# Kernel tuning notes

Measured on AMD Instinct MI355X. Metric: run time of the kernel, lower is better.

Reference implementation:

```python
import jax, jax.numpy as jnp
import numpy as np
import math

DIM = 512
NUM_HEADS = 8
DIM_HEAD = DIM // NUM_HEADS


def normalized_coords(h, w):
    # (h*w, 2) with (x, y) in [0, 1]
    y = jnp.linspace(0.0, 1.0, h)
    x = jnp.linspace(0.0, 1.0, w)
    yg, xg = jnp.meshgrid(y, x, indexing='ij')
    return jnp.stack([xg.ravel(), yg.ravel()], axis=-1)


def rotate_half(x):
    dh = x.shape[-1] // 2
    return jnp.concatenate([-x[..., dh:], x[..., :dh]], axis=-1)


def apply_rope(t, coords):
    # t: (n, heads, seq, dim_head); coords: (seq, 2) (identical across batch)
    dim_half = t.shape[-1] // 2
    freq = 1.0 / (10000.0 ** (jnp.arange(dim_half, dtype=jnp.float32) / dim_half))
    ang_x = coords[:, 0:1] * freq  # (seq, dim_half)
    ang_y = coords[:, 1:2] * freq
    ang = jnp.concatenate([ang_x, ang_y], axis=-1)  # (seq, dim_head)
    cos, sin = jnp.cos(ang), jnp.sin(ang)
    return t * cos + rotate_half(t) * sin


def setup_inputs() -> dict:
    key = jax.random.key(0)
    ks = jax.random.split(key, 12)
    n, Np, d, H, W = 4, 1024, DIM, 64, 64
    s = 0.02
    return {
        'local_feat': jax.random.normal(ks[0], (n, Np, d), jnp.float32),
        'global_feat': jax.random.normal(ks[1], (n, d, H, W), jnp.float32),
        'Wq': jax.random.normal(ks[2], (d, d), jnp.float32) * s,
        'bq': jnp.zeros((d,), jnp.float32),
        'Wk': jax.random.normal(ks[3], (d, d), jnp.float32) * s,
        'bk': jnp.zeros((d,), jnp.float32),
        'Wv': jax.random.normal(ks[4], (d, d), jnp.float32) * s,
        'bv': jnp.zeros((d,), jnp.float32),
        'Wg': jax.random.normal(ks[5], (d, 2 * d), jnp.float32) * s,
        'bg': jnp.zeros((d,), jnp.float32),
        'Wo': jax.random.normal(ks[6], (d, d), jnp.float32) * s,
        'bo': jnp.zeros((d,), jnp.float32),
    }


def reference(local_feat, global_feat, Wq, bq, Wk, bk, Wv, bv, Wg, bg, Wo, bo):
    n, Np, d = local_feat.shape
    _, _, H, W = global_feat.shape
    h, dh = NUM_HEADS, DIM_HEAD
    gf = global_feat.reshape(n, d, H * W).transpose(0, 2, 1)  # (n, HW, d)

    P = int(math.isqrt(Np))
    local_coords = normalized_coords(P, P)      # (Np, 2)
    global_coords = normalized_coords(H, W)     # (HW, 2)

    def proj(x, Wt, b):
        return x @ Wt.T + b

    Q = proj(local_feat, Wq, bq).reshape(n, Np, h, dh).transpose(0, 2, 1, 3)
    K = proj(gf, Wk, bk).reshape(n, H * W, h, dh).transpose(0, 2, 1, 3)
    V = proj(gf, Wv, bv).reshape(n, H * W, h, dh).transpose(0, 2, 1, 3)

    Q = apply_rope(Q, local_coords)
    K = apply_rope(K, global_coords)

    scores = jnp.einsum('bhqd,bhkd->bhqk', Q, K) / math.sqrt(dh)
    attn = jax.nn.softmax(scores, axis=-1)
    ao = jnp.einsum('bhqk,bhkd->bhqd', attn, V)
    ao = ao.transpose(0, 2, 1, 3).reshape(n, Np, d)

    gate = jax.nn.sigmoid(jnp.concatenate([local_feat, ao], axis=-1) @ Wg.T + bg)
    enhanced = local_feat + gate * ao
    return enhanced @ Wo.T + bo
```

## Files before the change

### kernel.cpp

```cpp
#include <hip/hip_runtime.h>
#include <hip/hip_bf16.h>
#include <cstdint>

typedef __hip_bfloat16 BF;
typedef unsigned short ushort_t;
typedef __attribute__((ext_vector_type(8))) __bf16 bf16x8;
typedef __attribute__((ext_vector_type(4))) float f32x4;
typedef __attribute__((ext_vector_type(4))) unsigned uint4v;

__device__ __forceinline__ float bu2f(ushort_t u) {
  return __uint_as_float((unsigned)u << 16);
}
__device__ __forceinline__ unsigned pk2(float a, float b) {
  union { __hip_bfloat162 h; unsigned u; } c;
  c.h = __float22bfloat162_rn(make_float2(a, b));
  return c.u;
}
__device__ __forceinline__ unsigned short f2bu(float f) {
  union { BF b; unsigned short u; } c; c.b = __float2bfloat16(f); return c.u;
}
__device__ __forceinline__ float b2f(BF x) { return __bfloat162float(x); }
__device__ __forceinline__ void rd16f(const float* fp, ushort_t* out) {
#pragma unroll
  for (int j = 0; j < 16; j += 4) {
    float4 v = *(const float4*)(fp + j);
    ((unsigned*)out)[j / 2] = pk2(v.x, v.y);
    ((unsigned*)out)[j / 2 + 1] = pk2(v.z, v.w);
  }
}

#define QS 0.1803368801111f

__global__ __launch_bounds__(256) void prep_k(const float* __restrict__ local,
                                              const float* __restrict__ Wq,
                                              const float* __restrict__ Wk,
                                              const float* __restrict__ Wv,
                                              const float* __restrict__ Wg,
                                              const float* __restrict__ Wo,
                                              BF* __restrict__ localB,
                                              BF* __restrict__ WB) {
  size_t e = ((size_t)blockIdx.x * 256 + threadIdx.x) * 16;
  const float* src;
  BF* dst;
  if (e < 2097152) {
    src = local + e;  dst = localB + e;
  } else {
    size_t f = e - 2097152;
    dst = WB + f;
    if (f < 262144)        src = Wq + f;
    else if (f < 524288)   src = Wk + (f - 262144);
    else if (f < 786432)   src = Wv + (f - 524288);
    else if (f < 1310720)  src = Wg + (f - 786432);
    else                   src = Wo + (f - 1310720);
  }
  ushort_t vals[16];
  rd16f(src, vals);
  *(uint4*)dst = *(uint4*)&vals[0];
  *((uint4*)dst + 1) = *(uint4*)&vals[8];
}

__global__ __launch_bounds__(256) void pre_k(const float* __restrict__ local,
                                             const float* __restrict__ gfeat,
                                             const float* __restrict__ Wq,
                                             const float* __restrict__ bq,
                                             const BF* __restrict__ localB,
                                             const BF* __restrict__ WqB,
                                             BF* __restrict__ gfT,
                                             BF* __restrict__ Qb) {
  __shared__ __align__(16) ushort_t smem[2][64][72];
  const int t = threadIdx.x;
  if (blockIdx.x < 2048) {
    auto T = smem[0];
    const int g = blockIdx.x;
    const int bz = g & 3, mt = (g >> 2) & 63, kt = g >> 8;
    {
      int krow = t >> 2, mg = t & 3;
      ushort_t vals[16];
      rd16f(gfeat + (size_t)bz * 512 * 4096 + (size_t)(kt * 64 + krow) * 4096 +
                mt * 64 + mg * 16,
            vals);
#pragma unroll
      for (int j = 0; j < 16; ++j) T[mg * 16 + j][krow] = vals[j];
    }
    __syncthreads();
    int mrow = t >> 2, kg = t & 3;
    uint4 a = *(const uint4*)&T[mrow][kg * 16];
    uint4 b = *(const uint4*)&T[mrow][kg * 16 + 8];
    size_t o = ((size_t)bz * 4096 + mt * 64 + mrow) * 512 + kt * 64 + kg * 16;
    *(uint4*)&gfT[o] = a;
    *(uint4*)&gfT[o + 8] = b;
    return;
  }
  auto As = smem[0];
  auto Bs = smem[1];
  const int bx = blockIdx.x - 2048;
  const int m0 = (bx & 63) * 64, n0 = (bx >> 6) * 64;
  const int w = t >> 6, lane = t & 63;
  const int quad = lane >> 4, l16 = lane & 15;

  f32x4 acc[4] = {};
  for (int k0 = 0; k0 < 512; k0 += 64) {
    __syncthreads();
    {
      int row = t >> 2, cg = t & 3;
      int kg = k0 + cg * 16;
      if (WqB) {
        const uint4* pa = (const uint4*)(localB + (size_t)(m0 + row) * 512 + kg);
        *(uint4*)&As[row][cg * 16] = pa[0];
        *(uint4*)&As[row][cg * 16 + 8] = pa[1];
        const uint4* pb = (const uint4*)(WqB + (size_t)(n0 + row) * 512 + kg);
        *(uint4*)&Bs[row][cg * 16] = pb[0];
        *(uint4*)&Bs[row][cg * 16 + 8] = pb[1];
      } else {
        ushort_t vals[16];
        rd16f(local + (size_t)(m0 + row) * 512 + kg, vals);
        *(uint4*)&As[row][cg * 16] = *(uint4*)&vals[0];
        *(uint4*)&As[row][cg * 16 + 8] = *(uint4*)&vals[8];
        ushort_t bv[16];
        rd16f(Wq + (size_t)(n0 + row) * 512 + kg, bv);
        *(uint4*)&Bs[row][cg * 16] = *(uint4*)&bv[0];
        *(uint4*)&Bs[row][cg * 16 + 8] = *(uint4*)&bv[8];
      }
    }
    __syncthreads();
#pragma unroll
    for (int kc = 0; kc < 2; ++kc) {
      bf16x8 af = *(const bf16x8*)&As[w * 16 + l16][kc * 32 + quad * 8];
#pragma unroll
      for (int nt = 0; nt < 4; ++nt) {
        bf16x8 bfv = *(const bf16x8*)&Bs[nt * 16 + l16][kc * 32 + quad * 8];
        acc[nt] = __builtin_amdgcn_mfma_f32_16x16x32_bf16(af, bfv, acc[nt], 0, 0, 0);
      }
    }
  }
  const int head = n0 >> 6;
#pragma unroll
  for (int r = 0; r < 4; ++r) {
    int mg = m0 + w * 16 + quad * 4 + r;
    int bb = mg >> 10, qi = mg & 1023;
    float x = (float)(qi & 31) * (1.f / 31.f);
    float y = (float)(qi >> 5) * (1.f / 31.f);
    size_t base = (((size_t)bb * 8 + head) * 1024 + qi) * 64;
#pragma unroll
    for (int j = 0; j < 2; ++j) {
      int c0 = j * 16 + l16;
      float t0 = acc[j][r] + bq[head * 64 + c0];
      float t1 = acc[j + 2][r] + bq[head * 64 + c0 + 32];
      float fr = __expf((float)c0 * (-9.210340371976184f / 32.f));
      float ax = x * fr, ay = y * fr;
      Qb[base + c0] = __float2bfloat16((t0 * __cosf(ax) - t1 * __sinf(ax)) * QS);
      Qb[base + c0 + 32] = __float2bfloat16((t1 * __cosf(ay) + t0 * __sinf(ay)) * QS);
    }
  }
}

__global__ __launch_bounds__(256) void kv_k(const BF* __restrict__ gfT,
                                            const float* __restrict__ Wk,
                                            const float* __restrict__ Wv,
                                            const BF* __restrict__ WkB,
                                            const BF* __restrict__ WvB,
                                            const float* __restrict__ bk,
                                            const float* __restrict__ bv,
                                            BF* __restrict__ Kb,
                                            BF* __restrict__ VTb) {
  __shared__ __align__(16) ushort_t smem[2][128][72];
  auto As = smem[0];
  auto Bs = smem[1];
  const int tid = threadIdx.x;
  const int w = tid >> 6, lane = tid & 63;
  const int quad = lane >> 4, l16 = lane & 15;
  const int wm = w >> 1, wn = w & 1;
  const int g = blockIdx.x;
  const int a = g & 7, y = (g >> 3) & 7, bidx = g >> 6;
  const int m0 = ((bidx << 1) | (a & 1)) * 128;
  const int n0 = y * 128;
  const int bz = a >> 1;

  f32x4 acc[4][4] = {};
  for (int k0 = 0; k0 < 512; k0 += 64) {
    __syncthreads();
#pragma unroll
    for (int u = 0; u < 2; ++u) {
      int unit = tid + u * 256;
      int row = unit >> 2, cg = unit & 3;
      const uint4* p = (const uint4*)(gfT + ((size_t)bz * 4096 + m0 + row) * 512 +
                                      k0 + cg * 16);
      *(uint4*)&As[row][cg * 16] = p[0];
      *(uint4*)&As[row][cg * 16 + 8] = p[1];
    }
    if (WkB) {
      const BF* bb16 = (n0 >= 512) ? WvB : WkB;
      const int nb = (n0 >= 512) ? (n0 - 512) : n0;
#pragma unroll
      for (int u = 0; u < 2; ++u) {
        int unit = tid + u * 256;
        int row = unit >> 2, cg = unit & 3;
        const uint4* p = (const uint4*)(bb16 + (size_t)(nb + row) * 512 +
                                        k0 + cg * 16);
        *(uint4*)&Bs[row][cg * 16] = p[0];
        *(uint4*)&Bs[row][cg * 16 + 8] = p[1];
      }
    } else {
#pragma unroll
      for (int u = 0; u < 2; ++u) {
        int unit = tid + u * 256;
        int row = unit >> 2, cg = unit & 3;
        const float* bsrc = (n0 >= 512) ? Wv : Wk;
        size_t nrow = (n0 >= 512) ? (n0 - 512 + row) : (n0 + row);
        ushort_t vals[16];
        rd16f(bsrc + nrow * 512 + k0 + cg * 16, vals);
        *(uint4*)&Bs[row][cg * 16] = *(uint4*)&vals[0];
        *(uint4*)&Bs[row][cg * 16 + 8] = *(uint4*)&vals[8];
      }
    }
    __syncthreads();
#pragma unroll
    for (int kc = 0; kc < 2; ++kc) {
      bf16x8 af[4], bfv[4];
#pragma unroll
      for (int i = 0; i < 4; ++i) {
        af[i] = *(const bf16x8*)&As[wm * 64 + i * 16 + l16][kc * 32 + quad * 8];
        bfv[i] = *(const bf16x8*)&Bs[wn * 64 + i * 16 + l16][kc * 32 + quad * 8];
      }
#pragma unroll
      for (int mt = 0; mt < 4; ++mt)
#pragma unroll
        for (int nt = 0; nt < 4; ++nt)
          acc[mt][nt] = __builtin_amdgcn_mfma_f32_16x16x32_bf16(af[mt], bfv[nt], acc[mt][nt], 0, 0, 0);
    }
  }
  if (n0 < 512) {
    const int head = (n0 + wn * 64) >> 6;
#pragma unroll
    for (int mt = 0; mt < 4; ++mt)
#pragma unroll
      for (int r = 0; r < 4; ++r) {
        int pg = m0 + wm * 64 + mt * 16 + quad * 4 + r;
        float x = (float)(pg & 63) * (1.f / 63.f);
        float yy = (float)(pg >> 6) * (1.f / 63.f);
        size_t base = (((size_t)bz * 8 + head) * 4096 + pg) * 64;
#pragma unroll
        for (int j = 0; j < 2; ++j) {
          int c0 = j * 16 + l16;
          float t0 = acc[mt][j][r] + bk[head * 64 + c0];
          float t1 = acc[mt][j + 2][r] + bk[head * 64 + c0 + 32];
          float fr = __expf((float)c0 * (-9.210340371976184f / 32.f));
          float ax = x * fr, ay = yy * fr;
          Kb[base + c0] = __float2bfloat16(t0 * __cosf(ax) - t1 * __sinf(ax));
          Kb[base + c0 + 32] = __float2bfloat16(t1 * __cosf(ay) + t0 * __sinf(ay));
        }
      }
  } else {
    const int n0v = n0 - 512;
    __syncthreads();
    ushort_t (*T)[136] = (ushort_t(*)[136]) & smem[0][0][0];
#pragma unroll
    for (int mt = 0; mt < 4; ++mt)
#pragma unroll
      for (int nt = 0; nt < 4; ++nt)
#pragma unroll
        for (int r = 0; r < 4; ++r) {
          int n_l = wn * 64 + nt * 16 + l16;
          int m_l = wm * 64 + mt * 16 + quad * 4 + r;
          T[n_l][m_l] = f2bu(acc[mt][nt][r] + bv[n0v + n_l]);
        }
    __syncthreads();
    int row = tid >> 1, half = tid & 1;
    size_t gbase = (((size_t)bz * 8 + (n0v >> 6) + (row >> 6)) * 64 + (row & 63)) * 4096 +
                   m0 + half * 64;
    uint4* dst = (uint4*)(VTb + gbase);
    const uint4* src = (const uint4*)&T[row][half * 64];
#pragma unroll
    for (int j = 0; j < 8; ++j) dst[j] = src[j];
  }
}

template <int NS>
__global__ __launch_bounds__(256, 4) void attn_k(const BF* __restrict__ Q,
                                                 const BF* __restrict__ K,
                                                 const BF* __restrict__ VT,
                                                 BF* __restrict__ AO,
                                                 BF* __restrict__ Opart,
                                                 float* __restrict__ lpart) {
  __shared__ __align__(16) ushort_t Ks[2][64][64];
  __shared__ __align__(16) ushort_t VTs[2][64][64];

  const int tid = threadIdx.x;
  const int w = tid >> 6, lane = tid & 63;
  const int quad = lane >> 4, l16 = lane & 15;
  const int r3 = l16 & 7;
  const int sc0 = (quad ^ r3) << 3;
  const int sc1 = sc0 ^ 32;

  const int g = blockIdx.x;
  const int bh = g & 31;
  const int qt = (g >> 5) & 7;
  const int ks = g >> 8;
  const int b = bh >> 3, h = bh & 7;
  const int q0 = qt * 128 + w * 32;
  const int kspan = 4096 / NS, kbase = ks * kspan;

  bf16x8 qa[2][2];
#pragma unroll
  for (int qs = 0; qs < 2; ++qs) {
    const BF* qp = Q + (((size_t)bh << 10) + q0 + qs * 16 + l16) * 64 + quad * 8;
    qa[qs][0] = *(const bf16x8*)qp;
    qa[qs][1] = *(const bf16x8*)(qp + 32);
  }
  bf16x8 ones;
#pragma unroll
  for (int j = 0; j < 8; ++j) ones[j] = (__bf16)1.0f;

  const BF* Kp = K + (size_t)bh * 4096 * 64;
  const BF* VTp = VT + (size_t)bh * 64 * 4096;

  f32x4 o[2][4] = {};
  f32x4 ol[2] = {};

  const int srow = tid >> 2, scol = (tid & 3) * 16;
  const int ssc = ((2 * (tid & 3)) ^ (srow & 7)) << 3;
  int vcol[4];
  {
    const int s1 = (tid >> 1) & 1, s0v = tid & 1;
#pragma unroll
    for (int gq = 0; gq < 4; ++gq)
      vcol[gq] = (((s1 * 4 + gq) ^ (srow & 7)) << 3) + s0v * 4;
  }

#define STAGE_V(buf, v0, v1)                                   \
  {                                                            \
    uint2 t_;                                                  \
    t_.x = (v0).x; t_.y = (v0).y; *(uint2*)&VTs[buf][srow][vcol[0]] = t_; \
    t_.x = (v0).z; t_.y = (v0).w; *(uint2*)&VTs[buf][srow][vcol[1]] = t_; \
    t_.x = (v1).x; t_.y = (v1).y; *(uint2*)&VTs[buf][srow][vcol[2]] = t_; \
    t_.x = (v1).z; t_.y = (v1).w; *(uint2*)&VTs[buf][srow][vcol[3]] = t_; \
  }

  {
    const uint4* kp = (const uint4*)(Kp + (size_t)(kbase + srow) * 64 + scol);
    const uint4* vp = (const uint4*)(VTp + (size_t)srow * 4096 + kbase + scol);
    uint4 a = kp[0], bb = kp[1], c = vp[0], d = vp[1];
    *(uint4*)&Ks[0][srow][ssc] = a;  *(uint4*)&Ks[0][srow][ssc ^ 8] = bb;
    STAGE_V(0, c, d);
  }
  __syncthreads();

  const int nc = kspan / 64;
  for (int c = 0; c < nc; ++c) {
    const int cur = c & 1;
    uint4 nk0, nk1, nv0, nv1;
    const bool more = (c + 1 < nc);
    if (more) {
      const int c1 = kbase + (c + 1) * 64;
      const uint4* kp = (const uint4*)(Kp + (size_t)(c1 + srow) * 64 + scol);
      const uint4* vp = (const uint4*)(VTp + (size_t)srow * 4096 + c1 + scol);
      nk0 = kp[0]; nk1 = kp[1]; nv0 = vp[0]; nv1 = vp[1];
    }

    unsigned pa_u[2][2][4];
#pragma unroll
    for (int ct = 0; ct < 4; ++ct) {
      const int krow = ct * 16 + l16;
      bf16x8 kb0 = *(const bf16x8*)&Ks[cur][krow][sc0];
      bf16x8 kb1 = *(const bf16x8*)&Ks[cur][krow][sc1];
#pragma unroll
      for (int qs = 0; qs < 2; ++qs) {
        f32x4 s = {};
        __builtin_amdgcn_s_setprio(1);
        s = __builtin_amdgcn_mfma_f32_16x16x32_bf16(kb0, qa[qs][0], s, 0, 0, 0);
        s = __builtin_amdgcn_mfma_f32_16x16x32_bf16(kb1, qa[qs][1], s, 0, 0, 0);
        __builtin_amdgcn_s_setprio(0);
        pa_u[qs][ct >> 1][(ct & 1) * 2] =
            pk2(__builtin_exp2f(s[0]), __builtin_exp2f(s[1]));
        pa_u[qs][ct >> 1][(ct & 1) * 2 + 1] =
            pk2(__builtin_exp2f(s[2]), __builtin_exp2f(s[3]));
      }
    }
    bf16x8 pa[2][2];
#pragma unroll
    for (int qs = 0; qs < 2; ++qs)
#pragma unroll
      for (int kk = 0; kk < 2; ++kk) {
        uint4v u = {pa_u[qs][kk][0], pa_u[qs][kk][1], pa_u[qs][kk][2],
                    pa_u[qs][kk][3]};
        pa[qs][kk] = __builtin_bit_cast(bf16x8, u);
      }

    __builtin_amdgcn_s_setprio(1);
#pragma unroll
    for (int qs = 0; qs < 2; ++qs) {
      ol[qs] = __builtin_amdgcn_mfma_f32_16x16x32_bf16(ones, pa[qs][0], ol[qs], 0, 0, 0);
      ol[qs] = __builtin_amdgcn_mfma_f32_16x16x32_bf16(ones, pa[qs][1], ol[qs], 0, 0, 0);
    }
#pragma unroll
    for (int nt = 0; nt < 4; ++nt) {
      const int vrow = nt * 16 + l16;
      bf16x8 vb0 = *(const bf16x8*)&VTs[cur][vrow][sc0];
      bf16x8 vb1 = *(const bf16x8*)&VTs[cur][vrow][sc1];
#pragma unroll
      for (int qs = 0; qs < 2; ++qs) {
        o[qs][nt] = __builtin_amdgcn_mfma_f32_16x16x32_bf16(vb0, pa[qs][0], o[qs][nt], 0, 0, 0);
        o[qs][nt] = __builtin_amdgcn_mfma_f32_16x16x32_bf16(vb1, pa[qs][1], o[qs][nt], 0, 0, 0);
      }
    }
    __builtin_amdgcn_s_setprio(0);

    if (more) {
      *(uint4*)&Ks[cur ^ 1][srow][ssc] = nk0;
      *(uint4*)&Ks[cur ^ 1][srow][ssc ^ 8] = nk1;
      STAGE_V(cur ^ 1, nv0, nv1);
    }
    __syncthreads();
  }
#undef STAGE_V

#pragma unroll
  for (int qs = 0; qs < 2; ++qs) {
    int qg = q0 + qs * 16 + l16;
    if (NS == 1) {
      float invl = 1.f / ol[qs][0];
#pragma unroll
      for (int nt = 0; nt < 4; ++nt) {
        uint2 uu;
        uu.x = pk2(o[qs][nt][0] * invl, o[qs][nt][1] * invl);
        uu.y = pk2(o[qs][nt][2] * invl, o[qs][nt][3] * invl);
        *(uint2*)(AO + (((size_t)b << 10) + qg) * 512 + h * 64 + nt * 16 + quad * 4) = uu;
      }
    } else {
      if (quad == 0) lpart[ks * 32768 + (bh << 10) + qg] = ol[qs][0];
#pragma unroll
      for (int nt = 0; nt < 4; ++nt) {
        uint2 uu;
        uu.x = pk2(o[qs][nt][0], o[qs][nt][1]);
        uu.y = pk2(o[qs][nt][2], o[qs][nt][3]);
        *(uint2*)(Opart + (size_t)ks * 2097152 + (((size_t)bh << 10) + qg) * 64 +
                  nt * 16 + quad * 4) = uu;
      }
    }
  }
}

template <int NS>
__global__ __launch_bounds__(256) void gate_k(const float* __restrict__ local,
                                              const BF* __restrict__ localB,
                                              const BF* __restrict__ AO,
                                              const BF* __restrict__ Opart,
                                              const float* __restrict__ lpart,
                                              const float* __restrict__ Wg,
                                              const BF* __restrict__ WgB,
                                              const float* __restrict__ bg,
                                              BF* __restrict__ ENH) {
  __shared__ __align__(16) ushort_t As[64][72];
  __shared__ __align__(16) ushort_t Bs[64][72];
  const int tid = threadIdx.x;
  const int w = tid >> 6, lane = tid & 63;
  const int quad = lane >> 4, l16 = lane & 15;
  const int m0 = blockIdx.x * 64, n0 = blockIdx.y * 64;

  f32x4 acc[4] = {};
  float aosv[4][4];
  for (int k0 = 0; k0 < 1024; k0 += 64) {
    __syncthreads();
    {
      int row = tid >> 2, cg = tid & 3;
      int kg = k0 + cg * 16;
      ushort_t vals[16];
      if (kg < 512) {
        if (localB) {
          const uint4* p = (const uint4*)(localB + (size_t)(m0 + row) * 512 + kg);
          *(uint4*)&vals[0] = p[0]; *(uint4*)&vals[8] = p[1];
        } else {
          rd16f(local + (size_t)(m0 + row) * 512 + kg, vals);
        }
      } else {
        int c = kg - 512;
        int hh = c >> 6, dh0 = c & 63;
        int mg = m0 + row;
        size_t bq = (size_t)(((mg >> 10) * 8 + hh) << 10) + (mg & 1023);
        if (NS == 1) {
          const uint4* p = (const uint4*)(AO + (size_t)mg * 512 + c);
          *(uint4*)&vals[0] = p[0]; *(uint4*)&vals[8] = p[1];
        } else {
          float ls = 0.f;
#pragma unroll
          for (int s2 = 0; s2 < NS; ++s2) ls += lpart[s2 * 32768 + bq];
          float inv = 1.f / ls;
          float av[16] = {};
#pragma unroll
          for (int s2 = 0; s2 < NS; ++s2) {
            const ushort_t* op = (const ushort_t*)Opart + (size_t)s2 * 2097152 +
                                 bq * 64 + dh0;
            uint4 u0 = ((const uint4*)op)[0], u1 = ((const uint4*)op)[1];
            const ushort_t* pu = (const ushort_t*)&u0;
#pragma unroll
            for (int j = 0; j < 8; ++j) av[j] += bu2f(pu[j]);
            pu = (const ushort_t*)&u1;
#pragma unroll
            for (int j = 0; j < 8; ++j) av[8 + j] += bu2f(pu[j]);
          }
#pragma unroll
          for (int j = 0; j < 16; j += 2)
            ((unsigned*)vals)[j / 2] = pk2(av[j] * inv, av[j + 1] * inv);
        }
      }
      *(uint4*)&As[row][cg * 16] = *(uint4*)&vals[0];
      *(uint4*)&As[row][cg * 16 + 8] = *(uint4*)&vals[8];
      if (WgB) {
        const uint4* p = (const uint4*)(WgB + (size_t)(n0 + row) * 1024 + kg);
        *(uint4*)&Bs[row][cg * 16] = p[0];
        *(uint4*)&Bs[row][cg * 16 + 8] = p[1];
      } else {
        ushort_t bv[16];
        rd16f(Wg + (size_t)(n0 + row) * 1024 + kg, bv);
        *(uint4*)&Bs[row][cg * 16] = *(uint4*)&bv[0];
        *(uint4*)&Bs[row][cg * 16 + 8] = *(uint4*)&bv[8];
      }
    }
    __syncthreads();
    if (k0 == 512 + n0) {
#pragma unroll
      for (int r = 0; r < 4; ++r)
#pragma unroll
        for (int nt = 0; nt < 4; ++nt)
          aosv[r][nt] = bu2f(As[w * 16 + quad * 4 + r][nt * 16 + l16]);
    }
#pragma unroll
    for (int kc = 0; kc < 2; ++kc) {
      bf16x8 af = *(const bf16x8*)&As[w * 16 + l16][kc * 32 + quad * 8];
#pragma unroll
      for (int nt = 0; nt < 4; ++nt) {
        bf16x8 bfv = *(const bf16x8*)&Bs[nt * 16 + l16][kc * 32 + quad * 8];
        acc[nt] = __builtin_amdgcn_mfma_f32_16x16x32_bf16(af, bfv, acc[nt], 0, 0, 0);
      }
    }
  }
#pragma unroll
  for (int r = 0; r < 4; ++r) {
    int mg = m0 + w * 16 + quad * 4 + r;
#pragma unroll
    for (int nt = 0; nt < 4; ++nt) {
      int ng = n0 + nt * 16 + l16;
      size_t idx = (size_t)mg * 512 + ng;
      float gg = 1.f / (1.f + __expf(-(acc[nt][r] + bg[ng])));
      ENH[idx] = __float2bfloat16(local[idx] + gg * aosv[r][nt]);
    }
  }
}

__global__ __launch_bounds__(256) void out_k(const BF* __restrict__ ENH,
                                             const float* __restrict__ Wo,
                                             const BF* __restrict__ WoB,
                                             const float* __restrict__ bo,
                                             float* __restrict__ out) {
  __shared__ __align__(16) ushort_t As[64][72];
  __shared__ __align__(16) ushort_t Bs[64][72];
  const int tid = threadIdx.x;
  const int w = tid >> 6, lane = tid & 63;
  const int quad = lane >> 4, l16 = lane & 15;
  const int m0 = blockIdx.x * 64, n0 = blockIdx.y * 64;

  f32x4 acc[4] = {};
  for (int k0 = 0; k0 < 512; k0 += 64) {
    __syncthreads();
    {
      int row = tid >> 2, cg = tid & 3;
      int kg = k0 + cg * 16;
      const uint4* p = (const uint4*)(ENH + (size_t)(m0 + row) * 512 + kg);
      *(uint4*)&As[row][cg * 16] = p[0];
      *(uint4*)&As[row][cg * 16 + 8] = p[1];
      if (WoB) {
        const uint4* pb = (const uint4*)(WoB + (size_t)(n0 + row) * 512 + kg);
        *(uint4*)&Bs[row][cg * 16] = pb[0];
        *(uint4*)&Bs[row][cg * 16 + 8] = pb[1];
      } else {
        ushort_t bv[16];
        rd16f(Wo + (size_t)(n0 + row) * 512 + kg, bv);
        *(uint4*)&Bs[row][cg * 16] = *(uint4*)&bv[0];
        *(uint4*)&Bs[row][cg * 16 + 8] = *(uint4*)&bv[8];
      }
    }
    __syncthreads();
#pragma unroll
    for (int kc = 0; kc < 2; ++kc) {
      bf16x8 af = *(const bf16x8*)&As[w * 16 + l16][kc * 32 + quad * 8];
#pragma unroll
      for (int nt = 0; nt < 4; ++nt) {
        bf16x8 bfv = *(const bf16x8*)&Bs[nt * 16 + l16][kc * 32 + quad * 8];
        acc[nt] = __builtin_amdgcn_mfma_f32_16x16x32_bf16(af, bfv, acc[nt], 0, 0, 0);
      }
    }
  }
#pragma unroll
  for (int r = 0; r < 4; ++r) {
    int mg = m0 + w * 16 + quad * 4 + r;
#pragma unroll
    for (int nt = 0; nt < 4; ++nt) {
      int ng = n0 + nt * 16 + l16;
      out[(size_t)mg * 512 + ng] = acc[nt][r] + bo[ng];
    }
  }
}

extern "C" void kernel_launch(void* const* d_in, const int* in_sizes, int n_in,
                              void* d_out, int out_size, void* d_ws, size_t ws_size,
                              hipStream_t stream) {
  const float* local = (const float*)d_in[0];
  const float* gfeat = (const float*)d_in[1];
  const float* Wq = (const float*)d_in[2];
  const float* bq = (const float*)d_in[3];
  const float* Wk = (const float*)d_in[4];
  const float* bk = (const float*)d_in[5];
  const float* Wv = (const float*)d_in[6];
  const float* bv = (const float*)d_in[7];
  const float* Wg = (const float*)d_in[8];
  const float* bg = (const float*)d_in[9];
  const float* Wo = (const float*)d_in[10];
  const float* bo = (const float*)d_in[11];

  char* w = (char*)d_ws;
  BF* Qb = (BF*)w;            w += (size_t)2097152 * 2;
  BF* Kb = (BF*)w;            w += (size_t)8388608 * 2;
  BF* VTb = (BF*)w;           w += (size_t)8388608 * 2;
  BF* AO = (BF*)w;            w += (size_t)2097152 * 2;
  BF* gfT = (BF*)w;
  BF* Opart = (BF*)w;
  size_t baseOff = (size_t)(w - (char*)d_ws);
  BF* ENH = Qb;

  int NS = 1;
  if (baseOff + 4 * (4194304 + 131072) <= ws_size) NS = 4;
  else if (baseOff + 16777216 + 2 * 131072 <= ws_size) NS = 2;
  float* lpart = (float*)(w + (size_t)NS * 4194304);

  size_t xsize = (size_t)NS * (4194304 + 131072);
  if (xsize < 16777216) xsize = 16777216;
  BF* WB = (BF*)(w + xsize);
  BF* localB = WB + 1572864;
  bool useP = (baseOff + xsize + 3145728 + 4194304) <= ws_size;
  const BF *WqB = nullptr, *WkB = nullptr, *WvB = nullptr, *WgB = nullptr,
           *WoB = nullptr, *locB = nullptr;
  if (useP) {
    WqB = WB;            WkB = WB + 262144;  WvB = WB + 524288;
    WgB = WB + 786432;   WoB = WB + 1310720; locB = localB;
  }

  dim3 blk(256);
  if (useP)
    prep_k<<<dim3(896), blk, 0, stream>>>(local, Wq, Wk, Wv, Wg, Wo, localB, WB);
  pre_k<<<dim3(2560), blk, 0, stream>>>(local, gfeat, Wq, bq, locB, WqB, gfT, Qb);
  kv_k<<<dim3(1024), blk, 0, stream>>>(gfT, Wk, Wv, WkB, WvB, bk, bv, Kb, VTb);
  if (NS == 4) {
    attn_k<4><<<dim3(1024), blk, 0, stream>>>(Qb, Kb, VTb, AO, Opart, lpart);
    gate_k<4><<<dim3(64, 8), blk, 0, stream>>>(local, locB, AO, Opart, lpart, Wg, WgB, bg, ENH);
  } else if (NS == 2) {
    attn_k<2><<<dim3(512), blk, 0, stream>>>(Qb, Kb, VTb, AO, Opart, lpart);
    gate_k<2><<<dim3(64, 8), blk, 0, stream>>>(local, locB, AO, Opart, lpart, Wg, WgB, bg, ENH);
  } else {
    attn_k<1><<<dim3(256), blk, 0, stream>>>(Qb, Kb, VTb, AO, nullptr, nullptr);
    gate_k<1><<<dim3(64, 8), blk, 0, stream>>>(local, locB, AO, Opart, lpart, Wg, WgB, bg, ENH);
  }
  out_k<<<dim3(64, 8), blk, 0, stream>>>(ENH, Wo, WoB, bo, (float*)d_out);
}
```

Measured before the change: 239.7 us.

## Software-pipeline attention loop: overlap PV of previous chunk with QK of next

Restructures the attention inner loop so each iteration runs the P·V MFMAs for the previous key chunk, then the score MFMAs and exp2 for the current chunk. V tiles move to a triple-buffered shared array so the V tile still being read is not overwritten. The aim is to let the exp/pack VALU work interleave with independent MFMAs and hide the dependency stall between scores and PV. It costs an extra 8KB of LDS per block, which may reduce occupancy, and keeps pa registers live across iterations.

```diff
diff --git a/kernel.cpp b/kernel.cpp
--- a/kernel.cpp
+++ b/kernel.cpp
@@ -283,7 +283,7 @@
                                                  BF* __restrict__ Opart,
                                                  float* __restrict__ lpart) {
   __shared__ __align__(16) ushort_t Ks[2][64][64];
-  __shared__ __align__(16) ushort_t VTs[2][64][64];
+  __shared__ __align__(16) ushort_t VTs[3][64][64];
 
   const int tid = threadIdx.x;
   const int w = tid >> 6, lane = tid & 63;
@@ -345,9 +345,73 @@
   }
   __syncthreads();
 
+  bf16x8 pa[2][2];
+
+#define S_PHASE(KRD)                                                          \
+  {                                                                           \
+    unsigned pu[2][2][4];                                                     \
+    _Pragma("unroll") for (int ct = 0; ct < 4; ++ct) {                        \
+      const int krow = ct * 16 + l16;                                         \
+      bf16x8 kb0 = *(const bf16x8*)&Ks[KRD][krow][sc0];                       \
+      bf16x8 kb1 = *(const bf16x8*)&Ks[KRD][krow][sc1];                       \
+      _Pragma("unroll") for (int qs = 0; qs < 2; ++qs) {                      \
+        f32x4 s = {};                                                         \
+        s = __builtin_amdgcn_mfma_f32_16x16x32_bf16(kb0, qa[qs][0], s, 0, 0, 0); \
+        s = __builtin_amdgcn_mfma_f32_16x16x32_bf16(kb1, qa[qs][1], s, 0, 0, 0); \
+        pu[qs][ct >> 1][(ct & 1) * 2] =                                       \
+            pk2(__builtin_exp2f(s[0]), __builtin_exp2f(s[1]));                \
+        pu[qs][ct >> 1][(ct & 1) * 2 + 1] =                                   \
+            pk2(__builtin_exp2f(s[2]), __builtin_exp2f(s[3]));                \
+      }                                                                       \
+    }                                                                         \
+    _Pragma("unroll") for (int qs = 0; qs < 2; ++qs)                          \
+      _Pragma("unroll") for (int kk = 0; kk < 2; ++kk) {                      \
+        uint4v u = {pu[qs][kk][0], pu[qs][kk][1], pu[qs][kk][2],              \
+                    pu[qs][kk][3]};                                           \
+        pa[qs][kk] = __builtin_bit_cast(bf16x8, u);                           \
+      }                                                                       \
+  }
+
+#define PV_PHASE(VRD)                                                         \
+  {                                                                           \
+    _Pragma("unroll") for (int qs = 0; qs < 2; ++qs) {                        \
+      ol[qs] = __builtin_amdgcn_mfma_f32_16x16x32_bf16(ones, pa[qs][0], ol[qs], 0, 0, 0); \
+      ol[qs] = __builtin_amdgcn_mfma_f32_16x16x32_bf16(ones, pa[qs][1], ol[qs], 0, 0, 0); \
+    }                                                                         \
+    _Pragma("unroll") for (int nt = 0; nt < 4; ++nt) {                        \
+      const int vrow = nt * 16 + l16;                                         \
+      bf16x8 vb0 = *(const bf16x8*)&VTs[VRD][vrow][sc0];                      \
+      bf16x8 vb1 = *(const bf16x8*)&VTs[VRD][vrow][sc1];                      \
+      _Pragma("unroll") for (int qs = 0; qs < 2; ++qs) {                      \
+        o[qs][nt] = __builtin_amdgcn_mfma_f32_16x16x32_bf16(vb0, pa[qs][0], o[qs][nt], 0, 0, 0); \
+        o[qs][nt] = __builtin_amdgcn_mfma_f32_16x16x32_bf16(vb1, pa[qs][1], o[qs][nt], 0, 0, 0); \
+      }                                                                       \
+    }                                                                         \
+  }
+
   const int nc = kspan / 64;
-  for (int c = 0; c < nc; ++c) {
-    const int cur = c & 1;
+  {
+    uint4 nk0, nk1, nv0, nv1;
+    const bool more = (nc > 1);
+    if (more) {
+      const int c1 = kbase + 64;
+      const uint4* kp = (const uint4*)(Kp + (size_t)(c1 + srow) * 64 + scol);
+      const uint4* vp = (const uint4*)(VTp + (size_t)srow * 4096 + c1 + scol);
+      nk0 = kp[0]; nk1 = kp[1]; nv0 = vp[0]; nv1 = vp[1];
+    }
+    __builtin_amdgcn_s_setprio(1);
+    S_PHASE(0);
+    __builtin_amdgcn_s_setprio(0);
+    if (more) {
+      *(uint4*)&Ks[1][srow][ssc] = nk0;
+      *(uint4*)&Ks[1][srow][ssc ^ 8] = nk1;
+      STAGE_V(1, nv0, nv1);
+    }
+    __syncthreads();
+  }
+
+  int krd = 1, vrd = 0, vwr = 2;
+  for (int c = 1; c < nc; ++c) {
     uint4 nk0, nk1, nv0, nv1;
     const bool more = (c + 1 < nc);
     if (more) {
@@ -356,63 +420,24 @@
       const uint4* vp = (const uint4*)(VTp + (size_t)srow * 4096 + c1 + scol);
       nk0 = kp[0]; nk1 = kp[1]; nv0 = vp[0]; nv1 = vp[1];
     }
-
-    unsigned pa_u[2][2][4];
-#pragma unroll
-    for (int ct = 0; ct < 4; ++ct) {
-      const int krow = ct * 16 + l16;
-      bf16x8 kb0 = *(const bf16x8*)&Ks[cur][krow][sc0];
-      bf16x8 kb1 = *(const bf16x8*)&Ks[cur][krow][sc1];
-#pragma unroll
-      for (int qs = 0; qs < 2; ++qs) {
-        f32x4 s = {};
-        __builtin_amdgcn_s_setprio(1);
-        s = __builtin_amdgcn_mfma_f32_16x16x32_bf16(kb0, qa[qs][0], s, 0, 0, 0);
-        s = __builtin_amdgcn_mfma_f32_16x16x32_bf16(kb1, qa[qs][1], s, 0, 0, 0);
-        __builtin_amdgcn_s_setprio(0);
-        pa_u[qs][ct >> 1][(ct & 1) * 2] =
-            pk2(__builtin_exp2f(s[0]), __builtin_exp2f(s[1]));
-        pa_u[qs][ct >> 1][(ct & 1) * 2 + 1] =
-            pk2(__builtin_exp2f(s[2]), __builtin_exp2f(s[3]));
-      }
-    }
-    bf16x8 pa[2][2];
-#pragma unroll
-    for (int qs = 0; qs < 2; ++qs)
-#pragma unroll
-      for (int kk = 0; kk < 2; ++kk) {
-        uint4v u = {pa_u[qs][kk][0], pa_u[qs][kk][1], pa_u[qs][kk][2],
-                    pa_u[qs][kk][3]};
-        pa[qs][kk] = __builtin_bit_cast(bf16x8, u);
-      }
-
     __builtin_amdgcn_s_setprio(1);
-#pragma unroll
-    for (int qs = 0; qs < 2; ++qs) {
-      ol[qs] = __builtin_amdgcn_mfma_f32_16x16x32_bf16(ones, pa[qs][0], ol[qs], 0, 0, 0);
-      ol[qs] = __builtin_amdgcn_mfma_f32_16x16x32_bf16(ones, pa[qs][1], ol[qs], 0, 0, 0);
-    }
-#pragma unroll
-    for (int nt = 0; nt < 4; ++nt) {
-      const int vrow = nt * 16 + l16;
-      bf16x8 vb0 = *(const bf16x8*)&VTs[cur][vrow][sc0];
-      bf16x8 vb1 = *(const bf16x8*)&VTs[cur][vrow][sc1];
-#pragma unroll
-      for (int qs = 0; qs < 2; ++qs) {
-        o[qs][nt] = __builtin_amdgcn_mfma_f32_16x16x32_bf16(vb0, pa[qs][0], o[qs][nt], 0, 0, 0);
-        o[qs][nt] = __builtin_amdgcn_mfma_f32_16x16x32_bf16(vb1, pa[qs][1], o[qs][nt], 0, 0, 0);
-      }
-    }
+    PV_PHASE(vrd);
+    S_PHASE(krd);
     __builtin_amdgcn_s_setprio(0);
-
     if (more) {
-      *(uint4*)&Ks[cur ^ 1][srow][ssc] = nk0;
-      *(uint4*)&Ks[cur ^ 1][srow][ssc ^ 8] = nk1;
-      STAGE_V(cur ^ 1, nv0, nv1);
-    }
-    __syncthreads();
-  }
+      *(uint4*)&Ks[krd ^ 1][srow][ssc] = nk0;
+      *(uint4*)&Ks[krd ^ 1][srow][ssc ^ 8] = nk1;
+      STAGE_V(vwr, nv0, nv1);
+    }
+    __syncthreads();
+    krd ^= 1;
+    vrd = (vrd == 2) ? 0 : vrd + 1;
+    vwr = (vwr == 2) ? 0 : vwr + 1;
+  }
+  PV_PHASE(vrd);
 #undef STAGE_V
+#undef S_PHASE
+#undef PV_PHASE
 
 #pragma unroll
   for (int qs = 0; qs < 2; ++qs) {
```

Result: no change. 239.1 us (median of 2 runs) (-0.2%).
